# Kernel optimization log

Measured on AMD Instinct MI355X. Metric: run time of the kernel, lower is better.

## Reference

```python
import jax, jax.numpy as jnp
import numpy as np

NUM_AA = 20
NUM_PAIRS = NUM_AA * NUM_AA  # 400 k-spaced amino-acid pair buckets


def setup_inputs() -> dict:
    key = jax.random.key(0)
    k1, k2 = jax.random.split(key)
    B, L, D = 256, 2048, 64
    seq = jax.random.randint(k1, (B, L), 0, NUM_AA, dtype=jnp.int64 if jax.config.jax_enable_x64 else jnp.int32)
    emb = jax.random.normal(k2, (B, L, D), dtype=jnp.float32)
    return {"seq": seq, "emb": emb, "k": 3}


def reference(seq, emb, k):
    """Vectorized CKSAAP embedding code.

    seq: [B, L] int amino-acid indices in [0, 20)
    emb: [B, L, D] float per-residue embeddings
    Returns: [B, k+1, 20, 20, D] averaged pair embeddings, matching
    CKSAAP.return_CKSAAP_Emb_code applied to each sequence in the batch.
    """
    B, L = seq.shape
    D = emb.shape[-1]

    def per_seq(s, e):
        outs = []
        for t in range(k + 1):
            n = L - t - 1  # number of k-spaced pairs for this gap
            left = s[:n]
            right = s[t + 1 : t + 1 + n]
            idx = left * NUM_AA + right  # [n] pair bucket index
            vals = 0.5 * (e[:n] + e[t + 1 : t + 1 + n])  # [n, D]
            hist = jax.ops.segment_sum(vals, idx, num_segments=NUM_PAIRS)  # [400, D]
            outs.append((hist / float(n)).reshape(NUM_AA, NUM_AA, D))
        return jnp.stack(outs)  # [k+1, 20, 20, D]

    return jax.vmap(per_seq)(seq, emb)
```

## Files before the change

### kernel.cpp

```cpp
#include <hip/hip_runtime.h>
#include <hip/hip_bf16.h>

#define NUM_AA    20
#define NUM_PAIRS 400
#define DD        64
#define NT        512
#define NW        8
#define LMAX      2048

__global__ __launch_bounds__(NT, 8)
void cksaap_kernel(const int* __restrict__ seq,
                   const float* __restrict__ emb,
                   float* __restrict__ out,
                   int B, int L, int k)
{
    __shared__ int            s_seq[LMAX];
    __shared__ unsigned short s_idx[LMAX];
    __shared__ unsigned short s_ord[LMAX];
    __shared__ int            s_cnt[NUM_PAIRS];
    __shared__ int            s_off[NUM_PAIRS];
    __shared__ int            s_cur[NUM_PAIRS];
    __shared__ int            s_scan[NT];

    const int T   = k + 1;
    const int nwg = gridDim.x;
    const int i   = blockIdx.x;
    int b, t;
    if (nwg == 1024 && T == 4) {
        const int x = i & 7;
        const int s = i >> 3;
        t = s >> 5;
        b = x * 32 + (s & 31);
    } else {
        b = i / T; t = i % T;
    }

    const int tid  = threadIdx.x;
    const int lane = tid & 63;
    const int wave = tid >> 6;
    const int n    = L - t - 1;

    for (int j = tid; j < L; j += NT) s_seq[j] = seq[(size_t)b * L + j];
    if (tid < NUM_PAIRS) s_cnt[tid] = 0;
    __syncthreads();

    for (int j = tid; j < n; j += NT) {
        const int idx = s_seq[j] * NUM_AA + s_seq[j + t + 1];
        s_idx[j] = (unsigned short)idx;
        atomicAdd(&s_cnt[idx], 1);
    }
    __syncthreads();

    const int c0 = (tid < NUM_PAIRS) ? s_cnt[tid] : 0;
    s_scan[tid] = c0;
    __syncthreads();
    for (int off = 1; off < NT; off <<= 1) {
        int v = s_scan[tid];
        if (tid >= off) v += s_scan[tid - off];
        __syncthreads();
        s_scan[tid] = v;
        __syncthreads();
    }
    if (tid < NUM_PAIRS) {
        const int excl = s_scan[tid] - c0;
        s_off[tid] = excl;
        s_cur[tid] = excl;
    }
    __syncthreads();

    for (int j = tid; j < n; j += NT) {
        const int idx = s_idx[j];
        const int r   = atomicAdd(&s_cur[idx], 1);
        s_ord[r] = (unsigned short)j;
    }
    __syncthreads();

    const float  scale = 0.5f / (float)n;
    const float* embb  = emb + (size_t)b * L * DD;
    float*       outp  = out + ((size_t)b * T + t) * (size_t)(NUM_PAIRS * DD);

    for (int p = wave; p < NUM_PAIRS; p += NW) {
        const int base = s_off[p];
        const int cnt  = s_cnt[p];
        float acc = 0.0f;
        int m = 0;
        for (; m + 4 <= cnt; m += 4) {
            const int j0 = s_ord[base + m + 0];
            const int j1 = s_ord[base + m + 1];
            const int j2 = s_ord[base + m + 2];
            const int j3 = s_ord[base + m + 3];
            const float a0 = embb[(size_t)j0 * DD + lane];
            const float b0 = embb[(size_t)(j0 + t + 1) * DD + lane];
            const float a1 = embb[(size_t)j1 * DD + lane];
            const float b1 = embb[(size_t)(j1 + t + 1) * DD + lane];
            const float a2 = embb[(size_t)j2 * DD + lane];
            const float b2 = embb[(size_t)(j2 + t + 1) * DD + lane];
            const float a3 = embb[(size_t)j3 * DD + lane];
            const float b3 = embb[(size_t)(j3 + t + 1) * DD + lane];
            acc += (a0 + b0) + (a1 + b1) + ((a2 + b2) + (a3 + b3));
        }
        for (; m < cnt; ++m) {
            const int j = s_ord[base + m];
            acc += embb[(size_t)j * DD + lane] +
                   embb[(size_t)(j + t + 1) * DD + lane];
        }
        outp[(size_t)p * DD + lane] = acc * scale;
    }
}

extern "C" void kernel_launch(void* const* d_in, const int* in_sizes, int n_in,
                              void* d_out, int out_size, void* d_ws, size_t ws_size,
                              hipStream_t stream)
{
    const int*   seq = (const int*)d_in[0];
    const float* emb = (const float*)d_in[1];
    float*       out = (float*)d_out;

    const int B = 256;
    const int L = in_sizes[0] / B;
    const int k = out_size / (B * NUM_PAIRS * DD) - 1;

    cksaap_kernel<<<B * (k + 1), NT, 0, stream>>>(seq, emb, out, B, L, k);
}
```

Measured before the change: 300.4 us.

## Batch 50 pair buckets per wave with padded index table for memory-level parallelism

Each wave now owns a contiguous block of 50 pair buckets and walks them in lockstep over a padded per-bucket index table of up to 20 entries. Empty slots hold a sentinel that gathers row 0 with zero weight. Each inner iteration therefore issues about 100 independent gather loads, which targets the latency-bound serial gather loop. Buckets with more than 20 entries are finished in a fallback loop. The cost is 50 accumulators per thread and more LDS, so occupancy hint drops from 8 to 4, plus wasted loads for padded slots.

```diff
diff --git a/kernel.cpp b/kernel.cpp
--- a/kernel.cpp
+++ b/kernel.cpp
@@ -6,9 +6,12 @@
 #define DD        64
 #define NT        512
 #define NW        8
+#define BPW       50
 #define LMAX      2048
+#define MAXC      20
+#define SENT      0xFFFFu
 
-__global__ __launch_bounds__(NT, 8)
+__global__ __launch_bounds__(NT, 4)
 void cksaap_kernel(const int* __restrict__ seq,
                    const float* __restrict__ emb,
                    float* __restrict__ out,
@@ -17,6 +20,7 @@
     __shared__ int            s_seq[LMAX];
     __shared__ unsigned short s_idx[LMAX];
     __shared__ unsigned short s_ord[LMAX];
+    __shared__ unsigned short s_pad[NUM_PAIRS * MAXC];
     __shared__ int            s_cnt[NUM_PAIRS];
     __shared__ int            s_off[NUM_PAIRS];
     __shared__ int            s_cur[NUM_PAIRS];
@@ -75,36 +79,57 @@
     }
     __syncthreads();
 
+    for (int e = tid; e < NUM_PAIRS * MAXC; e += NT) {
+        const int p = e / MAXC;
+        const int m = e - p * MAXC;
+        const int c = s_cnt[p];
+        s_pad[e] = (m < c) ? s_ord[s_off[p] + m] : (unsigned short)SENT;
+    }
+    __syncthreads();
+
     const float  scale = 0.5f / (float)n;
     const float* embb  = emb + (size_t)b * L * DD;
     float*       outp  = out + ((size_t)b * T + t) * (size_t)(NUM_PAIRS * DD);
+    const int    p0    = wave * BPW;
+    const int    gap   = (t + 1) * DD;
 
-    for (int p = wave; p < NUM_PAIRS; p += NW) {
-        const int base = s_off[p];
-        const int cnt  = s_cnt[p];
-        float acc = 0.0f;
-        int m = 0;
-        for (; m + 4 <= cnt; m += 4) {
-            const int j0 = s_ord[base + m + 0];
-            const int j1 = s_ord[base + m + 1];
-            const int j2 = s_ord[base + m + 2];
-            const int j3 = s_ord[base + m + 3];
-            const float a0 = embb[(size_t)j0 * DD + lane];
-            const float b0 = embb[(size_t)(j0 + t + 1) * DD + lane];
-            const float a1 = embb[(size_t)j1 * DD + lane];
-            const float b1 = embb[(size_t)(j1 + t + 1) * DD + lane];
-            const float a2 = embb[(size_t)j2 * DD + lane];
-            const float b2 = embb[(size_t)(j2 + t + 1) * DD + lane];
-            const float a3 = embb[(size_t)j3 * DD + lane];
-            const float b3 = embb[(size_t)(j3 + t + 1) * DD + lane];
-            acc += (a0 + b0) + (a1 + b1) + ((a2 + b2) + (a3 + b3));
+    int c = (lane < BPW) ? s_cnt[p0 + lane] : 0;
+    #pragma unroll
+    for (int o = 32; o > 0; o >>= 1) c = max(c, __shfl_xor(c, o));
+    const int maxm = min(c, MAXC);
+
+    float acc[BPW];
+    #pragma unroll
+    for (int q = 0; q < BPW; ++q) acc[q] = 0.0f;
+
+    for (int m = 0; m < maxm; ++m) {
+        #pragma unroll
+        for (int q = 0; q < BPW; ++q) {
+            const unsigned int j = s_pad[(p0 + q) * MAXC + m];
+            const int   jv = (j == SENT) ? 0 : (int)j;
+            const float w  = (j == SENT) ? 0.0f : 1.0f;
+            const float a  = embb[(size_t)jv * DD + lane];
+            const float bb = embb[(size_t)jv * DD + gap + lane];
+            acc[q] += w * (a + bb);
         }
-        for (; m < cnt; ++m) {
-            const int j = s_ord[base + m];
-            acc += embb[(size_t)j * DD + lane] +
-                   embb[(size_t)(j + t + 1) * DD + lane];
+    }
+
+    #pragma unroll 1
+    for (int q = 0; q < BPW; ++q) {
+        const int cc = s_cnt[p0 + q];
+        if (cc > MAXC) {
+            const int base = s_off[p0 + q];
+            for (int m = MAXC; m < cc; ++m) {
+                const int j = s_ord[base + m];
+                acc[q] += embb[(size_t)j * DD + lane] +
+                          embb[(size_t)j * DD + gap + lane];
+            }
         }
-        outp[(size_t)p * DD + lane] = acc * scale;
+    }
+
+    #pragma unroll
+    for (int q = 0; q < BPW; ++q) {
+        outp[(size_t)(p0 + q) * DD + lane] = acc[q] * scale;
     }
 }
 
```

After: 443.3 us. 47.6% more time.
